# Kernel tuning notes

Measured on AMD Instinct MI355X. Metric: run time of the kernel, lower is better.

## Reference

```python
import jax, jax.numpy as jnp
import numpy as np

SMOOTH = 1.0
EPS = 1e-8
K_SKEL = 50  # soft_skel default; module's self.k is unused in forward


def _max_pool3d(x, w):
    # x: (b, c, D, H, W); w: 3-tuple window; stride 1, 'same'-style padding (k-1)//2
    window = (1, 1) + tuple(w)
    pad = [(0, 0), (0, 0)] + [((k - 1) // 2, (k - 1) // 2) for k in w]
    return jax.lax.reduce_window(x, -jnp.inf, jax.lax.max, window, (1,) * 5, pad)


def soft_erode(I):
    p1 = -_max_pool3d(-I, (3, 1, 1))
    p2 = -_max_pool3d(-I, (1, 3, 1))
    p3 = -_max_pool3d(-I, (1, 1, 3))
    return jnp.minimum(jnp.minimum(p1, p3), p2)


def soft_dilate(I):
    return _max_pool3d(I, (3, 3, 3))


def soft_open(I):
    return soft_dilate(soft_erode(I))


def soft_skel(img, k=K_SKEL):
    skel = jax.nn.relu(img - soft_open(img))

    @jax.checkpoint
    def body(carry, _):
        img, skel = carry
        img = soft_erode(img)
        delta = jax.nn.relu(img - soft_open(img))
        skel = skel + jax.nn.relu(delta - skel * delta)
        return (img, skel), None

    (_, skel), _ = jax.lax.scan(body, (img, skel), None, length=k)
    return skel


def setup_inputs() -> dict:
    key = jax.random.key(0)
    kx, ky = jax.random.split(key)
    shape = (2, 2, 80, 80, 80)
    x = jax.random.uniform(kx, shape, dtype=jnp.float32)
    y = jax.random.uniform(ky, shape, dtype=jnp.float32)
    return {"x": x, "y": y}


def reference(x, y):
    # batch_dice=False -> reduce over spatial axes only
    axes = (2, 3, 4)
    clp = soft_skel(x)
    cll = soft_skel(y)
    # shapes equal -> y_onehot is the soft target itself
    tp = jnp.sum(x * cll, axis=axes)             # (b, c)
    fn = jnp.sum((1.0 - x) * cll, axis=axes)
    tpc = jnp.sum(clp * y, axis=axes)
    fpc = jnp.sum(clp * (1.0 - y), axis=axes)
    clp2voll = (tpc + SMOOTH) / (tpc + fpc + SMOOTH)
    cll2volp = (tp + SMOOTH) / (tp + fn + SMOOTH)
    dc = 2.0 * clp2voll * cll2volp / (cll2volp + clp2voll + EPS)
    return 1.0 - dc.mean()  # do_bg=True -> no channel slicing
```

## Files before the change

kernel.cpp:

```cpp
#include <hip/hip_runtime.h>

#define DDIM 80
#define PLANE 6400
#define VOL 512000
#define HALFV 4
#define NVOL 8
#define NTOT (NVOL*VOL)

#define TY 10
#define CZ 5
#define NYT 8
#define NZC 16
#define NCH 20
#define RP 84
#define ER (TY + 2)
#define BLK 256
#define GRID (NVOL*NYT*NZC)

__device__ __forceinline__ float4 f4min(float4 a, float4 b) {
    return make_float4(fminf(a.x,b.x), fminf(a.y,b.y), fminf(a.z,b.z), fminf(a.w,b.w));
}
__device__ __forceinline__ float4 f4max(float4 a, float4 b) {
    return make_float4(fmaxf(a.x,b.x), fmaxf(a.y,b.y), fmaxf(a.z,b.z), fmaxf(a.w,b.w));
}
__device__ __forceinline__ int slotE(int v){ return (v + 9) % 3; }
__device__ __forceinline__ int slotH(int v){ return (v + 8) & 3; }
__device__ __forceinline__ float updf(float s, float d){ return s + fmaxf(d - s*d, 0.0f); }

struct EIn { float4 c, zA, zB, yA, yB; float lf, rt; };

template<bool FIRST, bool LASTK>
__global__ __launch_bounds__(BLK, 4) void iter_k(const float* __restrict__ xin,
                                                 const float* __restrict__ yin,
                                                 const float* __restrict__ a,
                                                 float* __restrict__ eout,
                                                 float* __restrict__ skel)
{
    __shared__ float E[3][ER][RP];
    __shared__ float H[4][ER][RP];

    const int b = blockIdx.x;
    const int v   = b >> 7;
    const int rem = b & 127;
    const int yt  = rem >> 4;
    const int zci = rem & 15;
    const int y0 = yt*TY;
    const int z0 = zci*CZ;

    const float* __restrict__ src =
        FIRST ? ((v < HALFV) ? (xin + v*VOL) : (yin + (v-HALFV)*VOL)) : (a + v*VOL);
    float* __restrict__ ev = LASTK ? nullptr : (eout + v*VOL);
    float* __restrict__ skv = skel + v*VOL;

    const int tid = threadIdx.x;
    const int r = tid / NCH;
    const int c = tid - r*NCH;
    const int x4 = 4*c;

    auto loadE = [&](int zs, EIn& e) {
        if (tid < ER*NCH) {
            const int gy  = y0 - 1 + r;
            const int gyc = min(max(gy, 0), DDIM-1);
            const int zcl = min(max(zs, 0), DDIM-1);
            const int zm = max(zcl-1, 0), zp = min(zcl+1, DDIM-1);
            const int ym = max(gyc-1, 0), yp = min(gyc+1, DDIM-1);
            const float* rc = src + zcl*PLANE + gyc*DDIM;
            e.c  = *(const float4*)(rc + x4);
            e.lf = rc[max(x4-1, 0)];
            e.rt = rc[min(x4+4, DDIM-1)];
            e.zA = *(const float4*)(src + zm*PLANE + gyc*DDIM + x4);
            e.zB = *(const float4*)(src + zp*PLANE + gyc*DDIM + x4);
            e.yA = *(const float4*)(src + zcl*PLANE + ym*DDIM + x4);
            e.yB = *(const float4*)(src + zcl*PLANE + yp*DDIM + x4);
        }
    };

    auto erodeCompute = [&](const EIn& e) -> float4 {
        float4 m;
        m.x = fminf(fminf(e.lf,  e.c.x), e.c.y);
        m.y = fminf(fminf(e.c.x, e.c.y), e.c.z);
        m.z = fminf(fminf(e.c.y, e.c.z), e.c.w);
        m.w = fminf(fminf(e.c.z, e.c.w), e.rt);
        return f4min(m, f4min(f4min(e.zA, e.zB), f4min(e.yA, e.yB)));
    };

    auto storeE = [&](int zs, const float4& m) {
        if (tid < ER*NCH) {
            *(float4*)&E[slotE(zs)][r][x4] = m;
            if constexpr (!LASTK) {
                if (r >= 1 && r <= TY && zs >= z0 && zs < z0 + CZ)
                    *(float4*)(ev + zs*PLANE + (y0 + r - 1)*DDIM + x4) = m;
            }
        }
    };

    auto hmaxStore = [&](int zs, const float4& m) {
        if (tid < ER*NCH) {
            const float* er = &E[slotE(zs)][r][0];
            const float lf = (c > 0)  ? er[x4-1] : m.x;
            const float rt = (c < 19) ? er[x4+4] : m.w;
            float4 h;
            h.x = fmaxf(fmaxf(lf,  m.x), m.y);
            h.y = fmaxf(fmaxf(m.x, m.y), m.z);
            h.z = fmaxf(fmaxf(m.y, m.z), m.w);
            h.w = fmaxf(fmaxf(m.z, m.w), rt);
            *(float4*)&H[slotH(zs)][r][x4] = h;
        }
    };

    auto loadD = [&](int z, float4& img, float4& sk) {
        if (tid < TY*NCH) {
            const int off = z*PLANE + (y0 + r)*DDIM + x4;
            img = *(const float4*)(src + off);
            if constexpr (!FIRST) sk = *(const float4*)(skv + off);
        }
    };

    auto dilateUpd = [&](int z, const float4& img, const float4& skin) {
        if (tid < TY*NCH) {
            const int ss[3] = {slotH(z-1), slotH(z), slotH(z+1)};
            float4 dm = make_float4(-1e30f, -1e30f, -1e30f, -1e30f);
#pragma unroll
            for (int s = 0; s < 3; ++s)
#pragma unroll
                for (int l = 0; l < 3; ++l)
                    dm = f4max(dm, *(const float4*)&H[ss[s]][r + l][x4]);

            float4 dl;
            dl.x = fmaxf(img.x - dm.x, 0.0f);
            dl.y = fmaxf(img.y - dm.y, 0.0f);
            dl.z = fmaxf(img.z - dm.z, 0.0f);
            dl.w = fmaxf(img.w - dm.w, 0.0f);
            float4 s;
            if constexpr (FIRST) {
                s = dl;
            } else {
                s = skin;
                s.x = updf(s.x, dl.x); s.y = updf(s.y, dl.y);
                s.z = updf(s.z, dl.z); s.w = updf(s.w, dl.w);
            }
            *(float4*)(skv + z*PLANE + (y0 + r)*DDIM + x4) = s;
        }
    };

    EIn eIn, eTmp;
    float4 mOld, mNew;
    float4 dImg, dSk, dImgN, dSkN;

    loadE(z0-1, eIn);
    mOld = erodeCompute(eIn);
    loadE(z0, eTmp);
    mNew = erodeCompute(eTmp);
    storeE(z0-1, mOld);
    storeE(z0,   mNew);
    loadE(z0+1, eIn);
    __syncthreads();
    hmaxStore(z0-1, mOld);
    hmaxStore(z0,   mNew);
    mOld = erodeCompute(eIn);
    storeE(z0+1, mOld);
    loadE(z0+2, eIn);
    loadD(z0, dImg, dSk);
    __syncthreads();

#pragma unroll
    for (int S = 0; S < CZ; ++S) {
        const int z = z0 + S;
        if (S <= CZ-3) loadE(z+3, eTmp);
        if (S <= CZ-2) { mNew = erodeCompute(eIn); storeE(z+2, mNew); }
        hmaxStore(z+1, mOld);
        if (S <= CZ-2) loadD(z+1, dImgN, dSkN);
        __syncthreads();
        dilateUpd(z, dImg, dSk);
        if (S <= CZ-2) { mOld = mNew; dImg = dImgN; dSk = dSkN; }
        if (S <= CZ-3) { eIn = eTmp; }
    }
}

__global__ __launch_bounds__(256) void reduce_k(const float* __restrict__ x,
                                                const float* __restrict__ y,
                                                const float* __restrict__ skel,
                                                float* __restrict__ partials) {
    const int blk = blockIdx.x;
    const int v = blk >> 8;
    const int sub = blk & 255;
    const int base4 = (v * VOL + sub * 2000) >> 2;
    const float4* x4 = (const float4*)x;
    const float4* y4 = (const float4*)y;
    const float4* clp4 = (const float4*)(skel);
    const float4* cll4 = (const float4*)(skel + HALFV * VOL);
    float s1 = 0, s2 = 0, s3 = 0, s4 = 0;
    for (int j = threadIdx.x; j < 500; j += 256) {
        const int i4 = base4 + j;
        const float4 xv = x4[i4];
        const float4 yv = y4[i4];
        const float4 cp = clp4[i4];
        const float4 cl = cll4[i4];
        s1 += xv.x*cl.x + xv.y*cl.y + xv.z*cl.z + xv.w*cl.w;
        s2 += cl.x + cl.y + cl.z + cl.w;
        s3 += cp.x*yv.x + cp.y*yv.y + cp.z*yv.z + cp.w*yv.w;
        s4 += cp.x + cp.y + cp.z + cp.w;
    }
    for (int off = 32; off > 0; off >>= 1) {
        s1 += __shfl_down(s1, off);
        s2 += __shfl_down(s2, off);
        s3 += __shfl_down(s3, off);
        s4 += __shfl_down(s4, off);
    }
    __shared__ float smm[4][4];
    const int wave = threadIdx.x >> 6;
    if ((threadIdx.x & 63) == 0) {
        smm[wave][0] = s1; smm[wave][1] = s2; smm[wave][2] = s3; smm[wave][3] = s4;
    }
    __syncthreads();
    if (threadIdx.x == 0) {
        float a0 = 0, a1 = 0, a2 = 0, a3 = 0;
        for (int w = 0; w < 4; ++w) { a0 += smm[w][0]; a1 += smm[w][1]; a2 += smm[w][2]; a3 += smm[w][3]; }
        partials[blk*4 + 0] = a0;
        partials[blk*4 + 1] = a1;
        partials[blk*4 + 2] = a2;
        partials[blk*4 + 3] = a3;
    }
}

__global__ void final_k(const float* __restrict__ p, float* __restrict__ out) {
    __shared__ float sums[16];
    const int t = threadIdx.x;
    if (t < 16) {
        const int v = t >> 2, k = t & 3;
        float acc = 0.0f;
        for (int b = 0; b < 256; ++b) acc += p[((v << 8) + b)*4 + k];
        sums[t] = acc;
    }
    __syncthreads();
    if (t == 0) {
        float acc = 0.0f;
        for (int v = 0; v < 4; ++v) {
            const float tp      = sums[v*4 + 0];
            const float sum_cll = sums[v*4 + 1];
            const float tpc     = sums[v*4 + 2];
            const float sum_clp = sums[v*4 + 3];
            const float fn  = sum_cll - tp;
            const float fpc = sum_clp - tpc;
            const float clp2voll = (tpc + 1.0f) / (tpc + fpc + 1.0f);
            const float cll2volp = (tp + 1.0f) / (tp + fn + 1.0f);
            acc += 2.0f * clp2voll * cll2volp / (cll2volp + clp2voll + 1e-8f);
        }
        out[0] = 1.0f - acc * 0.25f;
    }
}

extern "C" void kernel_launch(void* const* d_in, const int* in_sizes, int n_in,
                              void* d_out, int out_size, void* d_ws, size_t ws_size,
                              hipStream_t stream) {
    const float* x = (const float*)d_in[0];
    const float* y = (const float*)d_in[1];
    float* out = (float*)d_out;

    float* bufA = (float*)d_ws;
    float* bufB = bufA + NTOT;
    float* skel = bufB + NTOT;
    float* partials = skel + NTOT;

    iter_k<true, false><<<GRID, BLK, 0, stream>>>(x, y, nullptr, bufA, skel);
    for (int t = 1; t <= 49; ++t) {
        iter_k<false, false><<<GRID, BLK, 0, stream>>>(nullptr, nullptr, bufA, bufB, skel);
        float* tmp = bufA; bufA = bufB; bufB = tmp;
    }
    iter_k<false, true><<<GRID, BLK, 0, stream>>>(nullptr, nullptr, bufA, nullptr, skel);

    reduce_k<<<1024, 256, 0, stream>>>(x, y, skel, partials);
    final_k<<<1, 64, 0, stream>>>(partials, out);
}
```

Baseline: 834.0 us.

## Deepen erode-input prefetch and use LDS-only barriers in skeleton kernel

The z-plane pipeline in the fused erode/dilate kernel now keeps two erode inputs in flight using alternating register buffers, so global loads for z+4 are issued before the current plane is consumed. __syncthreads is replaced with an inline-asm barrier that waits only on LDS counters (lgkmcnt), so outstanding global loads are not drained at each barrier. This is meant to hide global memory latency behind the shared-memory stages. The cost is more live registers at a four-wave occupancy bound, and correctness now depends on the barrier not waiting for pending global loads.

```diff
diff --git a/kernel.cpp b/kernel.cpp
--- a/kernel.cpp
+++ b/kernel.cpp
@@ -26,6 +26,10 @@
 __device__ __forceinline__ int slotE(int v){ return (v + 9) % 3; }
 __device__ __forceinline__ int slotH(int v){ return (v + 8) & 3; }
 __device__ __forceinline__ float updf(float s, float d){ return s + fmaxf(d - s*d, 0.0f); }
+
+__device__ __forceinline__ void lbar() {
+    asm volatile("s_waitcnt lgkmcnt(0)\n\ts_barrier" ::: "memory");
+}
 
 struct EIn { float4 c, zA, zB, yA, yB; float lf, rt; };
 
@@ -143,37 +147,39 @@
         }
     };
 
-    EIn eIn, eTmp;
-    float4 mOld, mNew;
+    EIn eP, eQ, eR;
+    float4 m0, m1, m2, mPrev, mNew;
     float4 dImg, dSk, dImgN, dSkN;
 
-    loadE(z0-1, eIn);
-    mOld = erodeCompute(eIn);
-    loadE(z0, eTmp);
-    mNew = erodeCompute(eTmp);
-    storeE(z0-1, mOld);
-    storeE(z0,   mNew);
-    loadE(z0+1, eIn);
-    __syncthreads();
-    hmaxStore(z0-1, mOld);
-    hmaxStore(z0,   mNew);
-    mOld = erodeCompute(eIn);
-    storeE(z0+1, mOld);
-    loadE(z0+2, eIn);
+    loadE(z0-1, eP);
+    loadE(z0,   eQ);
+    loadE(z0+1, eR);
+    m0 = erodeCompute(eP);  storeE(z0-1, m0);
+    m1 = erodeCompute(eQ);  storeE(z0,   m1);
+    lbar();
+
+    loadE(z0+2, eP);
+    loadE(z0+3, eQ);
+    hmaxStore(z0-1, m0);
+    hmaxStore(z0,   m1);
+    m2 = erodeCompute(eR);  storeE(z0+1, m2);
     loadD(z0, dImg, dSk);
-    __syncthreads();
+    lbar();
+    mPrev = m2;
 
 #pragma unroll
     for (int S = 0; S < CZ; ++S) {
         const int z = z0 + S;
-        if (S <= CZ-3) loadE(z+3, eTmp);
-        if (S <= CZ-2) { mNew = erodeCompute(eIn); storeE(z+2, mNew); }
-        hmaxStore(z+1, mOld);
+        if (S <= CZ-2) {
+            mNew = erodeCompute((S & 1) ? eQ : eP);
+            storeE(z+2, mNew);
+        }
+        if (S <= CZ-4) loadE(z+4, (S & 1) ? eQ : eP);
+        hmaxStore(z+1, mPrev);
         if (S <= CZ-2) loadD(z+1, dImgN, dSkN);
-        __syncthreads();
+        lbar();
         dilateUpd(z, dImg, dSk);
-        if (S <= CZ-2) { mOld = mNew; dImg = dImgN; dSk = dSkN; }
-        if (S <= CZ-3) { eIn = eTmp; }
+        if (S <= CZ-2) { mPrev = mNew; dImg = dImgN; dSk = dSkN; }
     }
 }
 
```

Result: no change. 845.3 us (+1.4%).
